# Kernel tuning notes

Measured on AMD Instinct MI355X. Metric: run time of the kernel, lower is better.

Reference implementation:

```python
import jax, jax.numpy as jnp
import numpy as np

N_TRIALS, T, INPUT_DIM = 32, 512, 64
N, R, OUTPUT_DIM = 4096, 8, 64
DT = 0.1


def setup_inputs() -> dict:
    key = jax.random.key(0)
    k_inp, k_B, k_W, k_m, k_n = jax.random.split(key, 5)
    inp = jax.random.normal(k_inp, (N_TRIALS, T, INPUT_DIM), dtype=jnp.float32)
    B = jax.random.normal(k_B, (N, INPUT_DIM), dtype=jnp.float32)
    W = jax.random.normal(k_W, (OUTPUT_DIM, N), dtype=jnp.float32) / np.sqrt(N)
    m = jax.random.normal(k_m, (N, R), dtype=jnp.float32)
    n = jax.random.normal(k_n, (N, R), dtype=jnp.float32)
    return {"inp": inp, "B": B, "W": W, "m": m, "n": n}


def reference(inp, B, W, m, n):
    # inp: [b, t, i]; B: [N, i]; W: [o, N]; m, n: [N, r]
    n_trials = inp.shape[0]
    # Precompute input projection for all steps: [t, b, N]
    inp_proj = jnp.einsum('bti,ni->tbn', inp, B)

    def step(x, u):
        # x: [b, N] voltage; u: [b, N] projected input at this step
        # sigmoid(x) @ (m n^T / N)^T == ((sigmoid(x) @ n) @ m^T) / N
        rec = (jax.nn.sigmoid(x) @ n) @ m.T / N
        x_new = (1.0 - DT) * x + DT * (rec + u)
        y = jax.nn.sigmoid(x_new) @ W.T  # [b, o]
        return x_new, (x_new, y)

    x0 = jnp.zeros((n_trials, N), dtype=inp.dtype)
    _, (xs, ys) = jax.lax.scan(step, x0, inp_proj)
    # xs: [t, b, N]; ys: [t, b, o]
    x_seq = jnp.concatenate([x0[None], xs], axis=0).transpose(1, 0, 2)  # [b, t+1, N]
    output_seq = ys.transpose(1, 0, 2)  # [b, t, o]
    return (x_seq, output_seq)
```

## Files before the change

kernel.cpp:

```cpp
#include <hip/hip_runtime.h>

static constexpr int BTRIALS = 32;
static constexpr int TSTEPS  = 512;
static constexpr int IDIM    = 64;
static constexpr int NDIM    = 4096;
static constexpr int RDIM    = 8;
static constexpr int ODIM    = 64;

typedef short v8s __attribute__((ext_vector_type(8)));
typedef float v4f __attribute__((ext_vector_type(4)));

__device__ __forceinline__ float fast_sigmoid(float x) {
    float e = __builtin_amdgcn_exp2f(x * -1.44269504088896340736f);
    return __builtin_amdgcn_rcpf(1.0f + e);
}

template <int CTRL, int RMASK>
__device__ __forceinline__ float dpp_add(float v) {
    int moved = __builtin_amdgcn_update_dpp(0, __float_as_int(v), CTRL, RMASK, 0xf, true);
    return v + __int_as_float(moved);
}

__device__ __forceinline__ float wave_reduce_to_lane63(float v) {
    v = dpp_add<0x111, 0xf>(v);
    v = dpp_add<0x112, 0xf>(v);
    v = dpp_add<0x114, 0xf>(v);
    v = dpp_add<0x118, 0xf>(v);
    v = dpp_add<0x142, 0xa>(v);
    v = dpp_add<0x143, 0xc>(v);
    return v;
}

__device__ __forceinline__ short f2bf(float f) {
    unsigned u = __float_as_uint(f);
    u += 0x7FFFu + ((u >> 16) & 1u);
    return (short)(u >> 16);
}

__global__ __launch_bounds__(256) void pre_gemm(const float* __restrict__ inp,
                                                const float* __restrict__ Bm,
                                                float* __restrict__ u,
                                                int t0, int rows) {
    __shared__ __align__(16) float At[64][68];
    __shared__ __align__(16) float Bt[64][68];
    const int tid = threadIdx.x;
    const int c4  = (tid & 15) * 4;
    const int rq  = tid >> 4;
    const int mbase = blockIdx.x * 64;
    const int nbase = blockIdx.y * 64;

    #pragma unroll
    for (int rr = 0; rr < 4; ++rr) {
        const int rloc = rr * 16 + rq;
        const int mr = mbase + rloc;
        float4 a = make_float4(0.f, 0.f, 0.f, 0.f);
        if (mr < rows) {
            const int b  = mr & 31;
            const int tl = mr >> 5;
            a = *(const float4*)(inp + ((size_t)b * TSTEPS + (t0 + tl)) * IDIM + c4);
        }
        At[c4 + 0][rloc] = a.x; At[c4 + 1][rloc] = a.y;
        At[c4 + 2][rloc] = a.z; At[c4 + 3][rloc] = a.w;
        const int n = nbase + rloc;
        float4 bb = *(const float4*)(Bm + (size_t)n * IDIM + c4);
        Bt[c4 + 0][rloc] = bb.x; Bt[c4 + 1][rloc] = bb.y;
        Bt[c4 + 2][rloc] = bb.z; Bt[c4 + 3][rloc] = bb.w;
    }
    __syncthreads();

    const int m4 = (tid >> 4) * 4;
    const int n4 = (tid & 15) * 4;
    float acc[4][4];
    #pragma unroll
    for (int i = 0; i < 4; ++i)
        #pragma unroll
        for (int j = 0; j < 4; ++j) acc[i][j] = 0.f;

    #pragma unroll 8
    for (int k = 0; k < 64; ++k) {
        float4 a = *(const float4*)&At[k][m4];
        float4 w = *(const float4*)&Bt[k][n4];
        float av[4] = {a.x, a.y, a.z, a.w};
        float wv[4] = {w.x, w.y, w.z, w.w};
        #pragma unroll
        for (int i = 0; i < 4; ++i)
            #pragma unroll
            for (int j = 0; j < 4; ++j)
                acc[i][j] = fmaf(av[i], wv[j], acc[i][j]);
    }

    #pragma unroll
    for (int i = 0; i < 4; ++i) {
        const int mr = mbase + m4 + i;
        if (mr < rows) {
            float4 o = make_float4(acc[i][0] * 0.1f, acc[i][1] * 0.1f,
                                   acc[i][2] * 0.1f, acc[i][3] * 0.1f);
            *(float4*)(u + (size_t)mr * NDIM + nbase + n4) = o;
        }
    }
}

__global__ __launch_bounds__(256) void wconv(const float* __restrict__ W,
                                             unsigned short* __restrict__ Wb) {
    const int base = (blockIdx.x * 256 + threadIdx.x) * 8;
    float4 a = *(const float4*)(W + base);
    float4 b = *(const float4*)(W + base + 4);
    v8s o;
    o[0] = f2bf(a.x); o[1] = f2bf(a.y); o[2] = f2bf(a.z); o[3] = f2bf(a.w);
    o[4] = f2bf(b.x); o[5] = f2bf(b.y); o[6] = f2bf(b.z); o[7] = f2bf(b.w);
    *(v8s*)(Wb + base) = o;
}

__global__ __launch_bounds__(512, 2) void scan_kernel(const float* __restrict__ mmat,
                                                      const float* __restrict__ nmat,
                                                      const float* __restrict__ u,
                                                      float* __restrict__ xseq,
                                                      float* __restrict__ xstate,
                                                      unsigned short* __restrict__ sbuf,
                                                      int t0, int tc) {
    const int b    = blockIdx.x;
    const int tid  = threadIdx.x;
    const int j0   = tid * 8;
    const int lane = tid & 63;
    const int wv   = tid >> 6;

    __shared__ __align__(16) float wlds[2][64];

    float nm[8][8], mmr[8][8], x[8], s[8];
    const float4* np4 = (const float4*)(nmat + (size_t)j0 * RDIM);
    const float4* mp4 = (const float4*)(mmat + (size_t)j0 * RDIM);
    const float mscale = 0.1f / 4096.0f;
    #pragma unroll
    for (int j = 0; j < 8; ++j) {
        float4 a = np4[j * 2], c = np4[j * 2 + 1];
        nm[j][0] = a.x; nm[j][1] = a.y; nm[j][2] = a.z; nm[j][3] = a.w;
        nm[j][4] = c.x; nm[j][5] = c.y; nm[j][6] = c.z; nm[j][7] = c.w;
        float4 d = mp4[j * 2], e = mp4[j * 2 + 1];
        mmr[j][0] = d.x * mscale; mmr[j][1] = d.y * mscale;
        mmr[j][2] = d.z * mscale; mmr[j][3] = d.w * mscale;
        mmr[j][4] = e.x * mscale; mmr[j][5] = e.y * mscale;
        mmr[j][6] = e.z * mscale; mmr[j][7] = e.w * mscale;
    }

    if (t0 == 0) {
        #pragma unroll
        for (int j = 0; j < 8; ++j) x[j] = 0.0f;
        float* z = xseq + (size_t)b * (TSTEPS + 1) * NDIM + j0;
        *(float4*)(z + 0) = make_float4(0.f, 0.f, 0.f, 0.f);
        *(float4*)(z + 4) = make_float4(0.f, 0.f, 0.f, 0.f);
    } else {
        const float* xs = xstate + (size_t)b * NDIM + j0;
        float4 v0 = *(const float4*)(xs + 0);
        float4 v1 = *(const float4*)(xs + 4);
        x[0] = v0.x; x[1] = v0.y; x[2] = v0.z; x[3] = v0.w;
        x[4] = v1.x; x[5] = v1.y; x[6] = v1.z; x[7] = v1.w;
    }
    #pragma unroll
    for (int j = 0; j < 8; ++j) s[j] = fast_sigmoid(x[j]);

    float uv[8];
    {
        const float* up = u + ((size_t)0 * BTRIALS + b) * NDIM + j0;
        float4 v0 = *(const float4*)(up + 0);
        float4 v1 = *(const float4*)(up + 4);
        uv[0] = v0.x; uv[1] = v0.y; uv[2] = v0.z; uv[3] = v0.w;
        uv[4] = v1.x; uv[5] = v1.y; uv[6] = v1.z; uv[7] = v1.w;
    }

    for (int tl = 0; tl < tc; ++tl) {
        const int buf = tl & 1;
        const int tn = (tl + 1 < tc) ? (tl + 1) : tl;
        const float* upn = u + ((size_t)tn * BTRIALS + b) * NDIM + j0;
        float4 pf0 = *(const float4*)(upn + 0);
        float4 pf1 = *(const float4*)(upn + 4);

        float part[8];
        #pragma unroll
        for (int r = 0; r < 8; ++r) part[r] = 0.0f;
        #pragma unroll
        for (int j = 0; j < 8; ++j) {
            #pragma unroll
            for (int r = 0; r < 8; ++r) part[r] = fmaf(s[j], nm[j][r], part[r]);
        }
        #pragma unroll
        for (int r = 0; r < 8; ++r) part[r] = wave_reduce_to_lane63(part[r]);

        if (lane == 63) {
            #pragma unroll
            for (int r = 0; r < 8; ++r) wlds[buf][r * 8 + wv] = part[r];
        }

        float xd[8];
        #pragma unroll
        for (int j = 0; j < 8; ++j) xd[j] = fmaf(0.9f, x[j], uv[j]);

        __syncthreads();

        float v = wlds[buf][lane];
        v = dpp_add<0x111, 0xf>(v);
        v = dpp_add<0x112, 0xf>(v);
        v = dpp_add<0x114, 0xf>(v);

        float ps[8];
        #pragma unroll
        for (int r = 0; r < 8; ++r)
            ps[r] = __int_as_float(__builtin_amdgcn_readlane(__float_as_int(v), r * 8 + 7));

        float* xrow = xseq + ((size_t)b * (TSTEPS + 1) + (t0 + tl + 1)) * NDIM + j0;
        #pragma unroll
        for (int j = 0; j < 8; ++j) {
            float acc = xd[j];
            #pragma unroll
            for (int r = 0; r < 8; ++r) acc = fmaf(ps[r], mmr[j][r], acc);
            x[j] = acc;
        }
        *(float4*)(xrow + 0) = make_float4(x[0], x[1], x[2], x[3]);
        *(float4*)(xrow + 4) = make_float4(x[4], x[5], x[6], x[7]);

        #pragma unroll
        for (int j = 0; j < 8; ++j) s[j] = fast_sigmoid(x[j]);
        v8s sv;
        sv[0] = f2bf(s[0]); sv[1] = f2bf(s[1]); sv[2] = f2bf(s[2]); sv[3] = f2bf(s[3]);
        sv[4] = f2bf(s[4]); sv[5] = f2bf(s[5]); sv[6] = f2bf(s[6]); sv[7] = f2bf(s[7]);
        *(v8s*)(sbuf + ((size_t)b * tc + tl) * NDIM + j0) = sv;

        uv[0] = pf0.x; uv[1] = pf0.y; uv[2] = pf0.z; uv[3] = pf0.w;
        uv[4] = pf1.x; uv[5] = pf1.y; uv[6] = pf1.z; uv[7] = pf1.w;
    }

    float* xs = xstate + (size_t)b * NDIM + j0;
    *(float4*)(xs + 0) = make_float4(x[0], x[1], x[2], x[3]);
    *(float4*)(xs + 4) = make_float4(x[4], x[5], x[6], x[7]);
}

__global__ __launch_bounds__(256) void y_gemm(const unsigned short* __restrict__ sbuf,
                                              const unsigned short* __restrict__ Wb,
                                              float* __restrict__ yout,
                                              int t0, int tc) {
    const int tid  = threadIdx.x;
    const int lane = tid & 63;
    const int mt   = blockIdx.x * 4 + (tid >> 6);
    const int lm   = lane & 15;
    const int kq   = lane >> 4;

    const int tilesPerB = tc >> 4;
    const int b  = mt / tilesPerB;
    const int tt = mt % tilesPerB;

    const unsigned short* pa = sbuf + ((size_t)b * tc + tt * 16 + lm) * NDIM + kq * 8;
    const unsigned short* pw = Wb + (size_t)lm * NDIM + kq * 8;

    v4f acc[4];
    #pragma unroll
    for (int ot = 0; ot < 4; ++ot) acc[ot] = (v4f){0.f, 0.f, 0.f, 0.f};

    #pragma unroll 4
    for (int kc = 0; kc < NDIM; kc += 32) {
        v8s af = *(const v8s*)(pa + kc);
        #pragma unroll
        for (int ot = 0; ot < 4; ++ot) {
            v8s bf = *(const v8s*)(pw + (size_t)ot * 16 * NDIM + kc);
            acc[ot] = __builtin_amdgcn_mfma_f32_16x16x32_bf16(af, bf, acc[ot], 0, 0, 0);
        }
    }

    #pragma unroll
    for (int ot = 0; ot < 4; ++ot) {
        #pragma unroll
        for (int r = 0; r < 4; ++r) {
            const int row = b * TSTEPS + t0 + tt * 16 + kq * 4 + r;
            yout[(size_t)row * ODIM + ot * 16 + lm] = acc[ot][r];
        }
    }
}

extern "C" void kernel_launch(void* const* d_in, const int* in_sizes, int n_in,
                              void* d_out, int out_size, void* d_ws, size_t ws_size,
                              hipStream_t stream) {
    const float* inp = (const float*)d_in[0];
    const float* Bm  = (const float*)d_in[1];
    const float* Wm  = (const float*)d_in[2];
    const float* mm  = (const float*)d_in[3];
    const float* nm  = (const float*)d_in[4];

    float* out  = (float*)d_out;
    float* xseq = out;
    float* yout = out + (size_t)BTRIALS * (TSTEPS + 1) * NDIM;

    float* xstate = (float*)d_ws;
    unsigned short* Wb = (unsigned short*)(xstate + (size_t)BTRIALS * NDIM);
    const size_t head = (size_t)BTRIALS * NDIM * sizeof(float)
                      + (size_t)ODIM * NDIM * sizeof(unsigned short);
    float* ubuf = (float*)((char*)d_ws + head);

    const size_t perstep = (size_t)BTRIALS * NDIM * (sizeof(float) + sizeof(unsigned short));
    size_t avail = (ws_size > head) ? (ws_size - head) : 0;
    int Tc = (int)(avail / perstep);
    if (Tc > TSTEPS) Tc = TSTEPS;
    Tc &= ~15;
    if (Tc < 16) Tc = 16;

    wconv<<<(ODIM * NDIM) / (256 * 8), 256, 0, stream>>>(Wm, Wb);

    for (int t0 = 0; t0 < TSTEPS; t0 += Tc) {
        const int tc = (TSTEPS - t0 < Tc) ? (TSTEPS - t0) : Tc;
        unsigned short* sbuf = (unsigned short*)(ubuf + (size_t)tc * BTRIALS * NDIM);
        const int rows = tc * BTRIALS;
        dim3 g1((rows + 63) / 64, NDIM / 64);
        pre_gemm<<<g1, 256, 0, stream>>>(inp, Bm, ubuf, t0, rows);
        scan_kernel<<<BTRIALS, 512, 0, stream>>>(mm, nm, ubuf, xseq, xstate, sbuf, t0, tc);
        const int mtiles = BTRIALS * (tc / 16);
        y_gemm<<<mtiles / 4, 256, 0, stream>>>(sbuf, Wb, yout, t0, tc);
    }
}
```

Measured before the change: 1.060 ms.

## Move input projection GEMM to bf16x3 split MFMA and use packed bf16 convert

Replaces the FP32 SIMT input-projection GEMM with an MFMA kernel. Inputs (pre-scaled by DT) and B are split into bf16 hi/lo pairs, and three products (hi*hi, hi*lo, lo*hi) are accumulated to stay close to FP32 accuracy. It also swaps the manual bf16 rounding of sigmoid outputs in the scan for the hardware packed v_cvt_pk_bf16_f32 instruction. This adds two conversion kernels and extra workspace for the split operands, which shrinks the space left for time chunks. The per-lane strided stores of u may be less coalesced than before.

```diff
diff --git a/kernel.cpp b/kernel.cpp
--- a/kernel.cpp
+++ b/kernel.cpp
@@ -37,67 +37,25 @@
     return (short)(u >> 16);
 }
 
-__global__ __launch_bounds__(256) void pre_gemm(const float* __restrict__ inp,
-                                                const float* __restrict__ Bm,
-                                                float* __restrict__ u,
-                                                int t0, int rows) {
-    __shared__ __align__(16) float At[64][68];
-    __shared__ __align__(16) float Bt[64][68];
-    const int tid = threadIdx.x;
-    const int c4  = (tid & 15) * 4;
-    const int rq  = tid >> 4;
-    const int mbase = blockIdx.x * 64;
-    const int nbase = blockIdx.y * 64;
-
-    #pragma unroll
-    for (int rr = 0; rr < 4; ++rr) {
-        const int rloc = rr * 16 + rq;
-        const int mr = mbase + rloc;
-        float4 a = make_float4(0.f, 0.f, 0.f, 0.f);
-        if (mr < rows) {
-            const int b  = mr & 31;
-            const int tl = mr >> 5;
-            a = *(const float4*)(inp + ((size_t)b * TSTEPS + (t0 + tl)) * IDIM + c4);
-        }
-        At[c4 + 0][rloc] = a.x; At[c4 + 1][rloc] = a.y;
-        At[c4 + 2][rloc] = a.z; At[c4 + 3][rloc] = a.w;
-        const int n = nbase + rloc;
-        float4 bb = *(const float4*)(Bm + (size_t)n * IDIM + c4);
-        Bt[c4 + 0][rloc] = bb.x; Bt[c4 + 1][rloc] = bb.y;
-        Bt[c4 + 2][rloc] = bb.z; Bt[c4 + 3][rloc] = bb.w;
-    }
-    __syncthreads();
-
-    const int m4 = (tid >> 4) * 4;
-    const int n4 = (tid & 15) * 4;
-    float acc[4][4];
-    #pragma unroll
-    for (int i = 0; i < 4; ++i)
-        #pragma unroll
-        for (int j = 0; j < 4; ++j) acc[i][j] = 0.f;
-
-    #pragma unroll 8
-    for (int k = 0; k < 64; ++k) {
-        float4 a = *(const float4*)&At[k][m4];
-        float4 w = *(const float4*)&Bt[k][n4];
-        float av[4] = {a.x, a.y, a.z, a.w};
-        float wv[4] = {w.x, w.y, w.z, w.w};
-        #pragma unroll
-        for (int i = 0; i < 4; ++i)
-            #pragma unroll
-            for (int j = 0; j < 4; ++j)
-                acc[i][j] = fmaf(av[i], wv[j], acc[i][j]);
-    }
-
-    #pragma unroll
-    for (int i = 0; i < 4; ++i) {
-        const int mr = mbase + m4 + i;
-        if (mr < rows) {
-            float4 o = make_float4(acc[i][0] * 0.1f, acc[i][1] * 0.1f,
-                                   acc[i][2] * 0.1f, acc[i][3] * 0.1f);
-            *(float4*)(u + (size_t)mr * NDIM + nbase + n4) = o;
-        }
-    }
+__global__ __launch_bounds__(256) void split_conv(const float* __restrict__ src,
+                                                  unsigned short* __restrict__ hi,
+                                                  unsigned short* __restrict__ lo,
+                                                  float scale) {
+    const int base = (blockIdx.x * 256 + threadIdx.x) * 8;
+    float4 a = *(const float4*)(src + base);
+    float4 b = *(const float4*)(src + base + 4);
+    float v[8] = {a.x, a.y, a.z, a.w, b.x, b.y, b.z, b.w};
+    v8s h, l;
+    #pragma unroll
+    for (int j = 0; j < 8; ++j) {
+        float f  = v[j] * scale;
+        short hb = f2bf(f);
+        h[j] = hb;
+        float fh = __uint_as_float(((unsigned)(unsigned short)hb) << 16);
+        l[j] = f2bf(f - fh);
+    }
+    *(v8s*)(hi + base) = h;
+    *(v8s*)(lo + base) = l;
 }
 
 __global__ __launch_bounds__(256) void wconv(const float* __restrict__ W,
@@ -109,6 +67,54 @@
     o[0] = f2bf(a.x); o[1] = f2bf(a.y); o[2] = f2bf(a.z); o[3] = f2bf(a.w);
     o[4] = f2bf(b.x); o[5] = f2bf(b.y); o[6] = f2bf(b.z); o[7] = f2bf(b.w);
     *(v8s*)(Wb + base) = o;
+}
+
+__global__ __launch_bounds__(256) void pre_gemm_mfma(const unsigned short* __restrict__ Ah,
+                                                     const unsigned short* __restrict__ Al,
+                                                     const unsigned short* __restrict__ Bh,
+                                                     const unsigned short* __restrict__ Bl,
+                                                     float* __restrict__ u, int t0) {
+    const int tid  = threadIdx.x;
+    const int lane = tid & 63;
+    const int wv   = tid >> 6;
+    const int lm   = lane & 15;
+    const int kq   = lane >> 4;
+
+    const int mloc = blockIdx.x * 16 + lm;
+    const int b    = mloc & 31;
+    const int t    = t0 + (mloc >> 5);
+    const size_t arow = (size_t)b * TSTEPS + t;
+
+    const unsigned short* pah = Ah + arow * IDIM + kq * 8;
+    const unsigned short* pal = Al + arow * IDIM + kq * 8;
+    v8s ah0 = *(const v8s*)(pah);
+    v8s ah1 = *(const v8s*)(pah + 32);
+    v8s al0 = *(const v8s*)(pal);
+    v8s al1 = *(const v8s*)(pal + 32);
+
+    const int n0   = wv * 1024;
+    const int urow = blockIdx.x * 16 + kq * 4;
+
+    #pragma unroll 2
+    for (int nt = 0; nt < 64; ++nt) {
+        const int n = n0 + nt * 16 + lm;
+        const unsigned short* pbh = Bh + (size_t)n * IDIM + kq * 8;
+        const unsigned short* pbl = Bl + (size_t)n * IDIM + kq * 8;
+        v8s bh0 = *(const v8s*)(pbh);
+        v8s bh1 = *(const v8s*)(pbh + 32);
+        v8s bl0 = *(const v8s*)(pbl);
+        v8s bl1 = *(const v8s*)(pbl + 32);
+        v4f acc = (v4f){0.f, 0.f, 0.f, 0.f};
+        acc = __builtin_amdgcn_mfma_f32_16x16x32_bf16(ah0, bl0, acc, 0, 0, 0);
+        acc = __builtin_amdgcn_mfma_f32_16x16x32_bf16(al0, bh0, acc, 0, 0, 0);
+        acc = __builtin_amdgcn_mfma_f32_16x16x32_bf16(ah1, bl1, acc, 0, 0, 0);
+        acc = __builtin_amdgcn_mfma_f32_16x16x32_bf16(al1, bh1, acc, 0, 0, 0);
+        acc = __builtin_amdgcn_mfma_f32_16x16x32_bf16(ah0, bh0, acc, 0, 0, 0);
+        acc = __builtin_amdgcn_mfma_f32_16x16x32_bf16(ah1, bh1, acc, 0, 0, 0);
+        float* up = u + (size_t)urow * NDIM + n0 + nt * 16 + lm;
+        #pragma unroll
+        for (int r = 0; r < 4; ++r) up[(size_t)r * NDIM] = acc[r];
+    }
 }
 
 __global__ __launch_bounds__(512, 2) void scan_kernel(const float* __restrict__ mmat,
@@ -219,10 +225,12 @@
 
         #pragma unroll
         for (int j = 0; j < 8; ++j) s[j] = fast_sigmoid(x[j]);
-        v8s sv;
-        sv[0] = f2bf(s[0]); sv[1] = f2bf(s[1]); sv[2] = f2bf(s[2]); sv[3] = f2bf(s[3]);
-        sv[4] = f2bf(s[4]); sv[5] = f2bf(s[5]); sv[6] = f2bf(s[6]); sv[7] = f2bf(s[7]);
-        *(v8s*)(sbuf + ((size_t)b * tc + tl) * NDIM + j0) = sv;
+        int c0, c1, c2, c3;
+        asm("v_cvt_pk_bf16_f32 %0, %1, %2" : "=v"(c0) : "v"(s[0]), "v"(s[1]));
+        asm("v_cvt_pk_bf16_f32 %0, %1, %2" : "=v"(c1) : "v"(s[2]), "v"(s[3]));
+        asm("v_cvt_pk_bf16_f32 %0, %1, %2" : "=v"(c2) : "v"(s[4]), "v"(s[5]));
+        asm("v_cvt_pk_bf16_f32 %0, %1, %2" : "=v"(c3) : "v"(s[6]), "v"(s[7]));
+        *(int4*)((void*)(sbuf + ((size_t)b * tc + tl) * NDIM + j0)) = make_int4(c0, c1, c2, c3);
 
         uv[0] = pf0.x; uv[1] = pf0.y; uv[2] = pf0.z; uv[3] = pf0.w;
         uv[4] = pf1.x; uv[5] = pf1.y; uv[6] = pf1.z; uv[7] = pf1.w;
@@ -287,12 +295,15 @@
     float* xseq = out;
     float* yout = out + (size_t)BTRIALS * (TSTEPS + 1) * NDIM;
 
-    float* xstate = (float*)d_ws;
+    float* xstate      = (float*)d_ws;
     unsigned short* Wb = (unsigned short*)(xstate + (size_t)BTRIALS * NDIM);
-    const size_t head = (size_t)BTRIALS * NDIM * sizeof(float)
-                      + (size_t)ODIM * NDIM * sizeof(unsigned short);
-    float* ubuf = (float*)((char*)d_ws + head);
-
+    unsigned short* Ah = Wb + (size_t)ODIM * NDIM;
+    unsigned short* Al = Ah + (size_t)BTRIALS * TSTEPS * IDIM;
+    unsigned short* Bh = Al + (size_t)BTRIALS * TSTEPS * IDIM;
+    unsigned short* Bl = Bh + (size_t)NDIM * IDIM;
+    float* ubuf        = (float*)(Bl + (size_t)NDIM * IDIM);
+
+    const size_t head = (size_t)((char*)ubuf - (char*)d_ws);
     const size_t perstep = (size_t)BTRIALS * NDIM * (sizeof(float) + sizeof(unsigned short));
     size_t avail = (ws_size > head) ? (ws_size - head) : 0;
     int Tc = (int)(avail / perstep);
@@ -301,13 +312,14 @@
     if (Tc < 16) Tc = 16;
 
     wconv<<<(ODIM * NDIM) / (256 * 8), 256, 0, stream>>>(Wm, Wb);
+    split_conv<<<(BTRIALS * TSTEPS * IDIM) / (256 * 8), 256, 0, stream>>>(inp, Ah, Al, 0.1f);
+    split_conv<<<(NDIM * IDIM) / (256 * 8), 256, 0, stream>>>(Bm, Bh, Bl, 1.0f);
 
     for (int t0 = 0; t0 < TSTEPS; t0 += Tc) {
         const int tc = (TSTEPS - t0 < Tc) ? (TSTEPS - t0) : Tc;
         unsigned short* sbuf = (unsigned short*)(ubuf + (size_t)tc * BTRIALS * NDIM);
         const int rows = tc * BTRIALS;
-        dim3 g1((rows + 63) / 64, NDIM / 64);
-        pre_gemm<<<g1, 256, 0, stream>>>(inp, Bm, ubuf, t0, rows);
+        pre_gemm_mfma<<<rows / 16, 256, 0, stream>>>(Ah, Al, Bh, Bl, ubuf, t0);
         scan_kernel<<<BTRIALS, 512, 0, stream>>>(mm, nm, ubuf, xseq, xstate, sbuf, t0, tc);
         const int mtiles = BTRIALS * (tc / 16);
         y_gemm<<<mtiles / 4, 256, 0, stream>>>(sbuf, Wb, yout, t0, tc);
```

Result: no change. 1.070 ms (+0.9%).
